# Kernel optimization log

Measured on AMD Instinct MI355X. Metric: run time of the kernel, lower is better.

Reference implementation:

```python
import jax, jax.numpy as jnp
import numpy as np

N_EMBD = 768
N_HEADS = 12

def setup_inputs() -> dict:
    key = jax.random.key(0)
    ks = jax.random.split(key, 5)
    B, T, C = 8, 1024, N_EMBD
    s_in = 1.0 / np.sqrt(C)
    x = jax.random.normal(ks[0], (B, T, C), dtype=jnp.float32)
    W_attn = jax.random.normal(ks[1], (C, 3 * C), dtype=jnp.float32) * s_in
    b_attn = jnp.zeros((3 * C,), dtype=jnp.float32)
    W_proj = jax.random.normal(ks[2], (C, C), dtype=jnp.float32) * s_in
    b_proj = jnp.zeros((C,), dtype=jnp.float32)
    return {"x": x, "W_attn": W_attn, "b_attn": b_attn, "W_proj": W_proj, "b_proj": b_proj}

def reference(x, W_attn, b_attn, W_proj, b_proj):
    B, T, C = x.shape
    H = N_HEADS
    hd = C // H
    qkv = x @ W_attn + b_attn                      # [B,T,3C]
    q, k, v = jnp.split(qkv, 3, axis=-1)
    # [B,T,C] -> [B,H,T,hd]
    q = q.reshape(B, T, H, hd).transpose(0, 2, 1, 3)
    k = k.reshape(B, T, H, hd).transpose(0, 2, 1, 3)
    v = v.reshape(B, T, H, hd).transpose(0, 2, 1, 3)
    att = jnp.einsum('bhqd,bhkd->bhqk', q, k) * (1.0 / np.sqrt(hd))
    mask = jnp.tril(jnp.ones((T, T), dtype=bool))
    att = jnp.where(mask, att, -jnp.inf)
    att = jax.nn.softmax(att, axis=-1)
    y = jnp.einsum('bhqk,bhkd->bhqd', att, v)      # [B,H,T,hd]
    y = y.transpose(0, 2, 1, 3).reshape(B, T, C)
    return y @ W_proj + b_proj
```

## Files before the change

kernel.cpp:

```cpp
#include <hip/hip_runtime.h>
#include <hip/hip_bf16.h>
#include <cmath>

typedef __bf16 bf16_t;
typedef __bf16 bf16x8 __attribute__((ext_vector_type(8)));
typedef float f32x4 __attribute__((ext_vector_type(4)));

#define MFMA16(A, B, C) __builtin_amdgcn_mfma_f32_16x16x32_bf16(A, B, C, 0, 0, 0)

#define GLOAD_LDS16(g, l)                                                      \
  __builtin_amdgcn_global_load_lds(                                            \
      (const __attribute__((address_space(1))) void*)(g),                      \
      (__attribute__((address_space(3))) void*)(l), 16, 0, 0)

__global__ __launch_bounds__(256) void prep(
    const float* __restrict__ x, bf16_t* __restrict__ xb,
    const float* __restrict__ Wa, bf16_t* __restrict__ wta,
    const float* __restrict__ Wp, bf16_t* __restrict__ wtp) {
  __shared__ bf16_t tile[32][33];
  const int id = blockIdx.x;
  if (id < 3072) {
    const size_t i = (size_t)id * 256 + threadIdx.x;
    const float4 a0 = ((const float4*)x)[i * 2];
    const float4 a1 = ((const float4*)x)[i * 2 + 1];
    bf16x8 v = {(bf16_t)a0.x, (bf16_t)a0.y, (bf16_t)a0.z, (bf16_t)a0.w,
                (bf16_t)a1.x, (bf16_t)a1.y, (bf16_t)a1.z, (bf16_t)a1.w};
    ((bf16x8*)xb)[i] = v;
    return;
  }
  const float* src;
  bf16_t* dst;
  int R, C, c0, r0;
  if (id < 3072 + 1728) {
    const int t = id - 3072;
    src = Wa; dst = wta; R = 768; C = 2304;
    c0 = (t % 72) * 32; r0 = (t / 72) * 32;
  } else {
    const int t = id - 4800;
    src = Wp; dst = wtp; R = 768; C = 768;
    c0 = (t % 24) * 32; r0 = (t / 24) * 32;
  }
  const int tr = threadIdx.x >> 5;
  const int tc = threadIdx.x & 31;
#pragma unroll
  for (int i = 0; i < 32; i += 8)
    tile[tr + i][tc] = (bf16_t)src[(size_t)(r0 + tr + i) * C + (c0 + tc)];
  __syncthreads();
#pragma unroll
  for (int i = 0; i < 32; i += 8)
    dst[(size_t)(c0 + tr + i) * R + (r0 + tc)] = tile[tc][tr + i];
}

__global__ __launch_bounds__(768, 1) void gemm_qkv(
    const bf16_t* __restrict__ A, const bf16_t* __restrict__ BT,
    const float* __restrict__ bias,
    bf16_t* __restrict__ o0, bf16_t* __restrict__ o1, bf16_t* __restrict__ o2,
    int K) {
  extern __shared__ __align__(16) bf16_t smem[];
  constexpr int ASZ = 256 * 64;
  constexpr int BSZ = 288 * 64;
  bf16_t* Bbase = smem + 2 * ASZ;

  const int tid = threadIdx.x;
  const int w = tid >> 6, lane = tid & 63;
  const int wr = w / 6, wc = w % 6;
  const int quad = lane >> 4, l16 = lane & 15;

  const int id = blockIdx.x;
  const int xcd = id & 7;
  const int lin = id >> 3;
  const int nt = lin & 7;
  const int mt = (xcd << 2) + (lin >> 3);

  const int dr = lane >> 3;
  const int dc = (((lane & 7) - dr) & 7) << 3;

  const int so0 = ((quad + (l16 & 7)) & 7) << 3;
  const int so1 = so0 ^ 32;

  f32x4 acc[8][3] = {};

  auto stage = [&](int t, int s) {
    const size_t ko = (size_t)t * 64 + dc;
#pragma unroll
    for (int j = 0; j < 6; ++j) {
      const int u = w + j * 12;
      if (u < 32) {
        GLOAD_LDS16(A + (size_t)(mt * 256 + u * 8 + dr) * K + ko,
                    smem + s * ASZ + u * 8 * 64);
      } else if (u < 68) {
        const int v = u - 32;
        GLOAD_LDS16(BT + (size_t)(nt * 288 + v * 8 + dr) * K + ko,
                    Bbase + s * BSZ + v * 8 * 64);
      }
    }
  };

  auto compute = [&](int s) {
#pragma unroll
    for (int ks = 0; ks < 2; ++ks) {
      const int so = ks ? so1 : so0;
      bf16x8 bfrag[3], afrag[8];
#pragma unroll
      for (int ni = 0; ni < 3; ++ni)
        bfrag[ni] = *(const bf16x8*)(Bbase + s * BSZ +
                                     (wc * 48 + ni * 16 + l16) * 64 + so);
#pragma unroll
      for (int mi = 0; mi < 8; ++mi)
        afrag[mi] = *(const bf16x8*)(smem + s * ASZ +
                                     (wr * 128 + mi * 16 + l16) * 64 + so);
      __builtin_amdgcn_s_setprio(1);
#pragma unroll
      for (int mi = 0; mi < 8; ++mi)
#pragma unroll
        for (int ni = 0; ni < 3; ++ni)
          acc[mi][ni] = MFMA16(afrag[mi], bfrag[ni], acc[mi][ni]);
      __builtin_amdgcn_s_setprio(0);
    }
  };

  const int NIT = K / 64;
  stage(0, 0);
  __syncthreads();
  for (int t = 0; t < NIT; ++t) {
    if (t + 1 < NIT) stage(t + 1, (t + 1) & 1);
    compute(t & 1);
    if (t + 1 < NIT) __syncthreads();
  }

  const int m_base = mt * 256 + wr * 128;
  const int n_base = nt * 288 + wc * 48;
#pragma unroll
  for (int ni = 0; ni < 3; ++ni) {
    const int n = n_base + ni * 16 + l16;
    const float bv = bias[n];
    const int which = n / 768;
    const int c = n - which * 768;
    const int h = c >> 6, d = c & 63;
#pragma unroll
    for (int mi = 0; mi < 8; ++mi) {
#pragma unroll
      for (int r = 0; r < 4; ++r) {
        const int m = m_base + mi * 16 + quad * 4 + r;
        const bf16_t bw = (bf16_t)(acc[mi][ni][r] + bv);
        const int b = m >> 10, t = m & 1023;
        const size_t bh = (size_t)(b * 12 + h);
        if (which == 0)
          o0[(bh * 1024 + t) * 64 + d] = bw;
        else if (which == 1)
          o1[(bh * 1024 + t) * 64 + d] = bw;
        else
          o2[(bh * 64 + d) * 1024 + t] = bw;
      }
    }
  }
}

__global__ __launch_bounds__(768, 1) void gemm_proj(
    const bf16_t* __restrict__ A, const bf16_t* __restrict__ BT,
    const float* __restrict__ bias, float* __restrict__ of, int N, int K) {
  extern __shared__ __align__(16) bf16_t smem[];
  constexpr int ASZ = 128 * 64;
  constexpr int BSZ = 192 * 64;
  bf16_t* Bbase = smem + 2 * ASZ;

  const int tid = threadIdx.x;
  const int w = tid >> 6, lane = tid & 63;
  const int wr = w / 6, wc = w % 6;
  const int quad = lane >> 4, l16 = lane & 15;

  const int id = blockIdx.x;
  const int xcd = id & 7;
  const int lin = id >> 3;
  const int nt = lin & 3;
  const int mt = (xcd << 3) + (lin >> 2);

  const int dr = lane >> 3;
  const int dc = (((lane & 7) - dr) & 7) << 3;

  const int so0 = ((quad + (l16 & 7)) & 7) << 3;
  const int so1 = so0 ^ 32;

  f32x4 acc[4][2] = {};

  auto stage = [&](int t, int s) {
    const size_t ko = (size_t)t * 64 + dc;
#pragma unroll
    for (int j = 0; j < 4; ++j) {
      const int u = w + j * 12;
      if (u < 16) {
        GLOAD_LDS16(A + (size_t)(mt * 128 + u * 8 + dr) * K + ko,
                    smem + s * ASZ + u * 8 * 64);
      } else if (u < 40) {
        const int v = u - 16;
        GLOAD_LDS16(BT + (size_t)(nt * 192 + v * 8 + dr) * K + ko,
                    Bbase + s * BSZ + v * 8 * 64);
      }
    }
  };

  auto compute = [&](int s) {
#pragma unroll
    for (int ks = 0; ks < 2; ++ks) {
      const int so = ks ? so1 : so0;
      bf16x8 bfrag[2], afrag[4];
#pragma unroll
      for (int ni = 0; ni < 2; ++ni)
        bfrag[ni] = *(const bf16x8*)(Bbase + s * BSZ +
                                     (wc * 32 + ni * 16 + l16) * 64 + so);
#pragma unroll
      for (int mi = 0; mi < 4; ++mi)
        afrag[mi] = *(const bf16x8*)(smem + s * ASZ +
                                     (wr * 64 + mi * 16 + l16) * 64 + so);
      __builtin_amdgcn_s_setprio(1);
#pragma unroll
      for (int mi = 0; mi < 4; ++mi)
#pragma unroll
        for (int ni = 0; ni < 2; ++ni)
          acc[mi][ni] = MFMA16(afrag[mi], bfrag[ni], acc[mi][ni]);
      __builtin_amdgcn_s_setprio(0);
    }
  };

  const int NIT = K / 64;
  stage(0, 0);
  __syncthreads();
  for (int t = 0; t < NIT; ++t) {
    if (t + 1 < NIT) stage(t + 1, (t + 1) & 1);
    compute(t & 1);
    if (t + 1 < NIT) __syncthreads();
  }

  const int m_base = mt * 128 + wr * 64;
  const int n_base = nt * 192 + wc * 32;
#pragma unroll
  for (int ni = 0; ni < 2; ++ni) {
    const int n = n_base + ni * 16 + l16;
    const float bv = bias[n];
#pragma unroll
    for (int mi = 0; mi < 4; ++mi)
#pragma unroll
      for (int r = 0; r < 4; ++r) {
        const int m = m_base + mi * 16 + quad * 4 + r;
        of[(size_t)m * N + n] = acc[mi][ni][r] + bv;
      }
  }
}

__global__ __launch_bounds__(256, 3) void attn_fwd(
    const bf16_t* __restrict__ Q, const bf16_t* __restrict__ Kg,
    const bf16_t* __restrict__ VT, bf16_t* __restrict__ Y) {
  __shared__ __align__(16) bf16_t Ks[2][64][64];
  __shared__ __align__(16) bf16_t Vs[2][64][64];
  __shared__ __align__(16) bf16_t Ps[4][16][72];

  const int tid = threadIdx.x;
  const int w = tid >> 6, lane = tid & 63;
  const int quad = lane >> 4, l16 = lane & 15;

  const int id = blockIdx.x;
  const int xcd = id & 7;
  const int lin = id >> 3;
  const int pair = lin & 7;
  const int h = lin >> 3;
  const int b = xcd;
  const size_t bh = (size_t)(b * 12 + h);
  const bf16_t* Qbh = Q + bh * 65536;
  const bf16_t* Kbh = Kg + bh * 65536;
  const bf16_t* VTbh = VT + bh * 65536;

  const int drow = lane >> 3;
  const int dchunk = (((lane & 7) - drow) & 7) << 3;

  const int so0 = ((quad + (l16 & 7)) & 7) << 3;
  const int so1 = so0 ^ 32;

  constexpr float SC = 0.18033688011112042f;
  constexpr float FM = 12.0f;
  const bf16_t one_b = (bf16_t)1.0f;
  const bf16x8 ones = {one_b, one_b, one_b, one_b,
                       one_b, one_b, one_b, one_b};

  auto stageKV = [&](int kt, int bufi) {
#pragma unroll
    for (int j = 0; j < 2; ++j) {
      const int r = w * 16 + j * 8 + drow;
      GLOAD_LDS16(Kbh + (size_t)(kt * 64 + r) * 64 + dchunk,
                  &Ks[bufi][w * 16 + j * 8][0]);
      GLOAD_LDS16(VTbh + (size_t)r * 1024 + kt * 64 + dchunk,
                  &Vs[bufi][w * 16 + j * 8][0]);
    }
  };

  const int qtb = 15 - pair;
  const int qts = pair;

  const int qrb = qtb * 64 + w * 16 + l16;
  const int qrs = qts * 64 + w * 16 + l16;
  const bf16x8 qb0 = *(const bf16x8*)(Qbh + (size_t)qrb * 64 + quad * 8);
  const bf16x8 qb1 = *(const bf16x8*)(Qbh + (size_t)qrb * 64 + 32 + quad * 8);
  const bf16x8 qs0 = *(const bf16x8*)(Qbh + (size_t)qrs * 64 + quad * 8);
  const bf16x8 qs1 = *(const bf16x8*)(Qbh + (size_t)qrs * 64 + 32 + quad * 8);

  f32x4 ob[5] = {};
  f32x4 os[5] = {};

  auto compute_q = [&](f32x4* o, const bf16x8& q0, const bf16x8& q1,
                       int bufi, bool diag) {
    f32x4 s[4];
#pragma unroll
    for (int ni = 0; ni < 4; ++ni) {
      bf16x8 kf0 = *(const bf16x8*)(&Ks[bufi][ni * 16 + l16][so0]);
      bf16x8 kf1 = *(const bf16x8*)(&Ks[bufi][ni * 16 + l16][so1]);
      f32x4 t = {};
      t = MFMA16(q0, kf0, t);
      t = MFMA16(q1, kf1, t);
      s[ni] = t;
    }
    if (diag) {
#pragma unroll
      for (int ni = 0; ni < 4; ++ni)
#pragma unroll
        for (int r = 0; r < 4; ++r) {
          const int kp = ni * 16 + l16;
          const int qr = w * 16 + quad * 4 + r;
          const float p = (kp > qr) ? 0.0f : exp2f(fmaf(s[ni][r], SC, -FM));
          Ps[w][quad * 4 + r][ni * 16 + l16] = (bf16_t)p;
        }
    } else {
#pragma unroll
      for (int ni = 0; ni < 4; ++ni)
#pragma unroll
        for (int r = 0; r < 4; ++r)
          Ps[w][quad * 4 + r][ni * 16 + l16] =
              (bf16_t)exp2f(fmaf(s[ni][r], SC, -FM));
    }
    bf16x8 pf0 = *(const bf16x8*)(&Ps[w][l16][quad * 8]);
    bf16x8 pf1 = *(const bf16x8*)(&Ps[w][l16][32 + quad * 8]);
#pragma unroll
    for (int nd = 0; nd < 4; ++nd) {
      bf16x8 vf0 = *(const bf16x8*)(&Vs[bufi][nd * 16 + l16][so0]);
      bf16x8 vf1 = *(const bf16x8*)(&Vs[bufi][nd * 16 + l16][so1]);
      o[nd] = MFMA16(pf0, vf0, o[nd]);
      o[nd] = MFMA16(pf1, vf1, o[nd]);
    }
    o[4] = MFMA16(pf0, ones, o[4]);
    o[4] = MFMA16(pf1, ones, o[4]);
  };

  stageKV(0, 0);
  int buf = 0;
  for (int kt = 0; kt <= qtb; ++kt) {
    __syncthreads();
    if (kt < qtb) stageKV(kt + 1, buf ^ 1);
    compute_q(ob, qb0, qb1, buf, kt == qtb);
    if (kt <= qts) compute_q(os, qs0, qs1, buf, kt == qts);
    buf ^= 1;
  }

#pragma unroll
  for (int r = 0; r < 4; ++r) {
    const float invb = 1.0f / ob[4][r];
    const int tb = qtb * 64 + w * 16 + quad * 4 + r;
    bf16_t* yb = Y + ((size_t)b * 1024 + tb) * 768 + h * 64;
#pragma unroll
    for (int nd = 0; nd < 4; ++nd)
      yb[nd * 16 + l16] = (bf16_t)(ob[nd][r] * invb);
    const float invs = 1.0f / os[4][r];
    const int ts = qts * 64 + w * 16 + quad * 4 + r;
    bf16_t* ys = Y + ((size_t)b * 1024 + ts) * 768 + h * 64;
#pragma unroll
    for (int nd = 0; nd < 4; ++nd)
      ys[nd * 16 + l16] = (bf16_t)(os[nd][r] * invs);
  }
}

extern "C" void kernel_launch(void* const* d_in, const int* in_sizes, int n_in,
                              void* d_out, int out_size, void* d_ws,
                              size_t ws_size, hipStream_t stream) {
  const float* x      = (const float*)d_in[0];
  const float* W_attn = (const float*)d_in[1];
  const float* b_attn = (const float*)d_in[2];
  const float* W_proj = (const float*)d_in[3];
  const float* b_proj = (const float*)d_in[4];
  float* out = (float*)d_out;

  const size_t HEADS = 96;
  bf16_t* wta = (bf16_t*)d_ws;
  bf16_t* wtp = wta + (size_t)2304 * 768;
  bf16_t* qw  = wtp + (size_t)768 * 768;
  bf16_t* kw  = qw + HEADS * 1024 * 64;
  bf16_t* vtw = kw + HEADS * 1024 * 64;
  bf16_t* yw  = vtw + HEADS * 1024 * 64;
  bf16_t* xb  = yw + (size_t)8192 * 768;

  prep<<<dim3(5376), 256, 0, stream>>>(x, xb, W_attn, wta, W_proj, wtp);
  const size_t qkv_lds = (size_t)(2 * (256 + 288) * 64) * sizeof(bf16_t);
  gemm_qkv<<<dim3(256), 768, qkv_lds, stream>>>(
      xb, wta, b_attn, qw, kw, vtw, 768);
  attn_fwd<<<dim3(768), 256, 0, stream>>>(qw, kw, vtw, yw);
  const size_t proj_lds = (size_t)(2 * (128 + 192) * 64) * sizeof(bf16_t);
  gemm_proj<<<dim3(256), 768, proj_lds, stream>>>(
      yw, wtp, b_proj, out, 768, 768);
}
```

Baseline: 190.4 us.

## Split QKV GEMM k-tiles into half-stages with finer barrier pipelining

Each 64-wide k-tile of the QKV GEMM is now loaded and consumed in two 32-wide halves, each with its own LDS plane and a new 4-way swizzle. Explicit vmcnt/lgkmcnt waits and raw s_barrier calls replace __syncthreads, so the prefetch of the next half overlaps the MFMA work on the current one. Register use drops because A fragments are loaded in two groups of four. The cost is more barriers per tile, a scratch region that absorbs dummy loads so every wave issues the same number of loads for uniform vmcnt accounting, and correctness that depends on the hand-written waitcnt counts.

```diff
diff --git a/kernel.cpp b/kernel.cpp
--- a/kernel.cpp
+++ b/kernel.cpp
@@ -57,9 +57,9 @@
     bf16_t* __restrict__ o0, bf16_t* __restrict__ o1, bf16_t* __restrict__ o2,
     int K) {
   extern __shared__ __align__(16) bf16_t smem[];
-  constexpr int ASZ = 256 * 64;
-  constexpr int BSZ = 288 * 64;
-  bf16_t* Bbase = smem + 2 * ASZ;
+  auto Apl = [&](int p, int h) { return smem + ((p * 2 + h) << 13); };
+  auto Bpl = [&](int p, int h) { return smem + 32768 + (p * 2 + h) * 9216; };
+  bf16_t* scratch = smem + 32768 + 36864;
 
   const int tid = threadIdx.x;
   const int w = tid >> 6, lane = tid & 63;
@@ -72,60 +72,85 @@
   const int nt = lin & 7;
   const int mt = (xcd << 2) + (lin >> 3);
 
-  const int dr = lane >> 3;
-  const int dc = (((lane & 7) - dr) & 7) << 3;
-
-  const int so0 = ((quad + (l16 & 7)) & 7) << 3;
-  const int so1 = so0 ^ 32;
+  const int rl = lane >> 2;
+  const int cq = ((lane & 3) - (rl >> 1)) & 3;
+  const int sw = ((quad + (l16 >> 1)) & 3) << 3;
 
   f32x4 acc[8][3] = {};
 
-  auto stage = [&](int t, int s) {
-    const size_t ko = (size_t)t * 64 + dc;
-#pragma unroll
-    for (int j = 0; j < 6; ++j) {
+  auto stage_half = [&](int t, int s, int h) {
+    const size_t ko = (size_t)t * 64 + h * 32 + cq * 8;
+#pragma unroll
+    for (int j = 0; j < 3; ++j) {
       const int u = w + j * 12;
-      if (u < 32) {
-        GLOAD_LDS16(A + (size_t)(mt * 256 + u * 8 + dr) * K + ko,
-                    smem + s * ASZ + u * 8 * 64);
-      } else if (u < 68) {
-        const int v = u - 32;
-        GLOAD_LDS16(BT + (size_t)(nt * 288 + v * 8 + dr) * K + ko,
-                    Bbase + s * BSZ + v * 8 * 64);
+      if (u < 16) {
+        GLOAD_LDS16(A + (size_t)(mt * 256 + u * 16 + rl) * K + ko,
+                    Apl(s, h) + u * 16 * 32);
+      } else if (u < 34) {
+        const int v = u - 16;
+        GLOAD_LDS16(BT + (size_t)(nt * 288 + v * 16 + rl) * K + ko,
+                    Bpl(s, h) + v * 16 * 32);
+      } else {
+        const int v = u - 34;
+        GLOAD_LDS16(BT + (size_t)(nt * 288 + v * 16 + rl) * K + ko,
+                    scratch + v * 512);
       }
     }
   };
 
-  auto compute = [&](int s) {
-#pragma unroll
-    for (int ks = 0; ks < 2; ++ks) {
-      const int so = ks ? so1 : so0;
-      bf16x8 bfrag[3], afrag[8];
+  bf16x8 bfr[3], af[4];
+  auto ldB = [&](int p, int h) {
+#pragma unroll
+    for (int ni = 0; ni < 3; ++ni)
+      bfr[ni] = *(const bf16x8*)(Bpl(p, h) +
+                                 (wc * 48 + ni * 16 + l16) * 32 + sw);
+  };
+  auto ldA = [&](int p, int h, int mh) {
+#pragma unroll
+    for (int mi = 0; mi < 4; ++mi)
+      af[mi] = *(const bf16x8*)(Apl(p, h) +
+                                (wr * 128 + mh * 64 + mi * 16 + l16) * 32 + sw);
+  };
+  auto mm12 = [&](int mh) {
+    __builtin_amdgcn_s_setprio(1);
+#pragma unroll
+    for (int mi = 0; mi < 4; ++mi)
 #pragma unroll
       for (int ni = 0; ni < 3; ++ni)
-        bfrag[ni] = *(const bf16x8*)(Bbase + s * BSZ +
-                                     (wc * 48 + ni * 16 + l16) * 64 + so);
-#pragma unroll
-      for (int mi = 0; mi < 8; ++mi)
-        afrag[mi] = *(const bf16x8*)(smem + s * ASZ +
-                                     (wr * 128 + mi * 16 + l16) * 64 + so);
-      __builtin_amdgcn_s_setprio(1);
-#pragma unroll
-      for (int mi = 0; mi < 8; ++mi)
-#pragma unroll
-        for (int ni = 0; ni < 3; ++ni)
-          acc[mi][ni] = MFMA16(afrag[mi], bfrag[ni], acc[mi][ni]);
-      __builtin_amdgcn_s_setprio(0);
-    }
+        acc[mh * 4 + mi][ni] = MFMA16(af[mi], bfr[ni], acc[mh * 4 + mi][ni]);
+    __builtin_amdgcn_s_setprio(0);
   };
 
   const int NIT = K / 64;
-  stage(0, 0);
-  __syncthreads();
+  stage_half(0, 0, 0);
+  stage_half(0, 0, 1);
+
   for (int t = 0; t < NIT; ++t) {
-    if (t + 1 < NIT) stage(t + 1, (t + 1) & 1);
-    compute(t & 1);
-    if (t + 1 < NIT) __syncthreads();
+    const int p = t & 1, nxt = p ^ 1;
+    const bool pf = (t + 1 < NIT);
+    asm volatile("s_waitcnt lgkmcnt(0)" ::: "memory");
+    asm volatile("s_waitcnt vmcnt(3)" ::: "memory");
+    __builtin_amdgcn_s_barrier();
+    asm volatile("" ::: "memory");
+    if (pf) stage_half(t + 1, nxt, 0);
+    ldB(p, 0);
+    ldA(p, 0, 0);
+    mm12(0);
+    ldA(p, 0, 1);
+    mm12(1);
+    asm volatile("s_waitcnt lgkmcnt(0)" ::: "memory");
+    if (pf)
+      asm volatile("s_waitcnt vmcnt(3)" ::: "memory");
+    else
+      asm volatile("s_waitcnt vmcnt(0)" ::: "memory");
+    __builtin_amdgcn_s_barrier();
+    asm volatile("" ::: "memory");
+    if (pf) stage_half(t + 1, nxt, 1);
+    ldB(p, 1);
+    ldA(p, 1, 0);
+    mm12(0);
+    ldA(p, 1, 1);
+    mm12(1);
   }
 
   const int m_base = mt * 256 + wr * 128;
@@ -395,7 +420,7 @@
   bf16_t* xb  = yw + (size_t)8192 * 768;
 
   prep<<<dim3(5376), 256, 0, stream>>>(x, xb, W_attn, wta, W_proj, wtp);
-  const size_t qkv_lds = (size_t)(2 * (256 + 288) * 64) * sizeof(bf16_t);
+  const size_t qkv_lds = (size_t)(32768 + 36864 + 1024) * sizeof(bf16_t);
   gemm_qkv<<<dim3(256), 768, qkv_lds, stream>>>(
       xb, wta, b_attn, qw, kw, vtw, 768);
   attn_fwd<<<dim3(768), 256, 0, stream>>>(qw, kw, vtw, yw);
```

Result: no change. 188.4 us (-1.1%).
